# Kernel tuning notes

Hardware: AMD Instinct MI355X
Metric: run time of the kernel (lower is better)

Reference implementation:

```python
import jax, jax.numpy as jnp
import numpy as np

IN_FEATURES = 2048
OUT_FEATURES = 8192
HARMONICS = 256
TWO_PI = 2.0 * np.pi


def setup_inputs() -> dict:
    key = jax.random.key(0)
    kx, kb, kp = jax.random.split(key, 3)
    x = jax.random.normal(kx, (4, 4096, IN_FEATURES), dtype=jnp.float32)
    # basis: randn then L2-normalized along in_features (dim=1), as in torch buffer init
    basis = jax.random.normal(kb, (HARMONICS, IN_FEATURES), dtype=jnp.float32)
    basis = basis / jnp.linalg.norm(basis, axis=1, keepdims=True)
    phase = jax.random.normal(kp, (OUT_FEATURES, HARMONICS), dtype=jnp.float32) * TWO_PI
    amp = jnp.ones((OUT_FEATURES, HARMONICS), dtype=jnp.float32) / HARMONICS
    return {"x": x, "basis": basis, "phase": phase, "amp": amp}


def reference(x, basis, phase, amp):
    # resonance = x @ basis.T : [..., harmonics]
    resonance = jnp.einsum("bsi,hi->bsh", x, basis)
    # Real part of (resonance + 0i) * (amp*cos(phase) + i*amp*sin(phase)) summed over h
    # collapses to resonance @ (amp * cos(phase)).T -- identical math, no complex dtype.
    w_real = amp * jnp.cos(phase)  # [out, harmonics]
    return jnp.einsum("bsh,oh->bso", resonance, w_real)
```

## Files before the change

### kernel.cpp

```cpp
#include <hip/hip_runtime.h>
#include <hip/hip_bf16.h>
#include <stdint.h>
#include <stddef.h>


typedef __bf16 bf16x8 __attribute__((ext_vector_type(8)));
typedef float  f32x4  __attribute__((ext_vector_type(4)));
typedef float  f32x16 __attribute__((ext_vector_type(16)));
typedef unsigned short u16x8 __attribute__((ext_vector_type(8)));

#define M_ROWS 16384
#define K_IN   2048
#define N_OUT  8192
#define N_HARM 256

__device__ inline unsigned short f2bf(float f) {
    union { float f; uint32_t u; } c; c.f = f;
    uint32_t u = c.u;
    uint32_t r = (u + 0x7fffu + ((u >> 16) & 1u)) >> 16;
    return (unsigned short)r;
}

__device__ inline bf16x8 cvt8(f32x4 a, f32x4 b) {
    bf16x8 r;
    r[0] = (__bf16)a[0]; r[1] = (__bf16)a[1]; r[2] = (__bf16)a[2]; r[3] = (__bf16)a[3];
    r[4] = (__bf16)b[0]; r[5] = (__bf16)b[1]; r[6] = (__bf16)b[2]; r[7] = (__bf16)b[3];
    return r;
}

#define GLDS(src, dst) \
    __builtin_amdgcn_global_load_lds((const __attribute__((address_space(1))) void*)(src), \
                                     (__attribute__((address_space(3))) void*)(dst), 16, 0, 0)

__global__ __launch_bounds__(256) void cvt_bf16(const float* __restrict__ in,
                                                unsigned short* __restrict__ out) {
    size_t i = ((size_t)blockIdx.x * 256 + threadIdx.x) * 8;
    f32x4 v0 = *(const f32x4*)(in + i);
    f32x4 v1 = *(const f32x4*)(in + i + 4);
    u16x8 o;
    o[0] = f2bf(v0[0]); o[1] = f2bf(v0[1]); o[2] = f2bf(v0[2]); o[3] = f2bf(v0[3]);
    o[4] = f2bf(v1[0]); o[5] = f2bf(v1[1]); o[6] = f2bf(v1[2]); o[7] = f2bf(v1[3]);
    *(u16x8*)(out + i) = o;
}

__global__ __launch_bounds__(256) void wreal_bf16(const float* __restrict__ phase,
                                                  const float* __restrict__ amp,
                                                  unsigned short* __restrict__ out) {
    size_t i = ((size_t)blockIdx.x * 256 + threadIdx.x) * 8;
    f32x4 p0 = *(const f32x4*)(phase + i);
    f32x4 p1 = *(const f32x4*)(phase + i + 4);
    f32x4 a0 = *(const f32x4*)(amp + i);
    f32x4 a1 = *(const f32x4*)(amp + i + 4);
    u16x8 o;
    o[0] = f2bf(a0[0] * cosf(p0[0])); o[1] = f2bf(a0[1] * cosf(p0[1]));
    o[2] = f2bf(a0[2] * cosf(p0[2])); o[3] = f2bf(a0[3] * cosf(p0[3]));
    o[4] = f2bf(a1[0] * cosf(p1[0])); o[5] = f2bf(a1[1] * cosf(p1[1]));
    o[6] = f2bf(a1[2] * cosf(p1[2])); o[7] = f2bf(a1[3] * cosf(p1[3]));
    *(u16x8*)(out + i) = o;
}

__global__ __launch_bounds__(256) void gemm1_fused(const float* __restrict__ A,
                                                   const unsigned short* __restrict__ B,
                                                   unsigned short* __restrict__ C) {
    __shared__ float          Asm[2][32 * 64];
    __shared__ unsigned short Bsm[2][256 * 64];

    const int tid  = threadIdx.x;
    const int lane = tid & 63;
    const int wv   = tid >> 6;
    const int bm0  = blockIdx.x * 32;

    const float* srcA[2];
#pragma unroll
    for (int q = 0; q < 2; ++q) {
        int L = q * 256 + tid;
        int r = L >> 4, p = L & 15;
        int c = p ^ (r & 15);
        srcA[q] = A + (size_t)(bm0 + r) * K_IN + c * 4;
    }
    const unsigned short* srcB[8];
#pragma unroll
    for (int q = 0; q < 8; ++q) {
        int L = q * 256 + tid;
        int r = L >> 3, p = L & 7;
        int c = p ^ (r & 7);
        srcB[q] = B + (size_t)r * K_IN + c * 8;
    }
    const int dA = wv * 256 + lane * 4;
    const int dB = wv * 512 + lane * 8;

    f32x16 acc[2];
#pragma unroll
    for (int nf = 0; nf < 2; ++nf)
#pragma unroll
        for (int e = 0; e < 16; ++e) acc[nf][e] = 0.f;

    const int r   = lane & 31;
    const int g   = lane >> 5;
    const int r15 = r & 15;
    const int colb = wv * 64;

#pragma unroll
    for (int q = 0; q < 2; ++q) GLDS(srcA[q], &Asm[0][q * 1024 + dA]);
#pragma unroll
    for (int q = 0; q < 8; ++q) GLDS(srcB[q], &Bsm[0][q * 2048 + dB]);
    __syncthreads();

    for (int t = 0; t < 32; ++t) {
        const int buf = t & 1;
        if (t + 1 < 32) {
            const int k0 = (t + 1) * 64;
#pragma unroll
            for (int q = 0; q < 2; ++q) GLDS(srcA[q] + k0, &Asm[buf ^ 1][q * 1024 + dA]);
#pragma unroll
            for (int q = 0; q < 8; ++q) GLDS(srcB[q] + k0, &Bsm[buf ^ 1][q * 2048 + dB]);
        }

        bf16x8 af[4];
#pragma unroll
        for (int ks = 0; ks < 4; ++ks) {
            const int c0 = g * 2 + ks * 4;
            f32x4 lo = *(const f32x4*)&Asm[buf][r * 64 + ((c0)     ^ r15) * 4];
            f32x4 hi = *(const f32x4*)&Asm[buf][r * 64 + ((c0 + 1) ^ r15) * 4];
            af[ks] = cvt8(lo, hi);
        }
#pragma unroll
        for (int nf = 0; nf < 2; ++nf) {
            const int rB = colb + nf * 32 + r;
            const int r7 = rB & 7;
#pragma unroll
            for (int ks = 0; ks < 4; ++ks) {
                const int cB = g + ks * 2;
                bf16x8 bfrag = *(const bf16x8*)&Bsm[buf][rB * 64 + (cB ^ r7) * 8];
                acc[nf] = __builtin_amdgcn_mfma_f32_32x32x16_bf16(af[ks], bfrag, acc[nf], 0, 0, 0);
            }
        }
        __syncthreads();
    }

#pragma unroll
    for (int nf = 0; nf < 2; ++nf)
#pragma unroll
        for (int reg = 0; reg < 16; ++reg) {
            int row = bm0 + (reg & 3) + 8 * (reg >> 2) + 4 * g;
            int col = colb + nf * 32 + r;
            C[(size_t)row * N_HARM + col] = f2bf(acc[nf][reg]);
        }
}

template<int K, int NCOLS>
__global__ __launch_bounds__(256) void gemm_bt(const unsigned short* __restrict__ A,
                                               const unsigned short* __restrict__ B,
                                               float* __restrict__ Cv) {
    __shared__ unsigned short As[2][128 * 32];
    __shared__ unsigned short Bs[2][128 * 32];

    const int tid  = threadIdx.x;
    const int lane = tid & 63;
    const int wv   = tid >> 6;
    const int wr   = wv >> 1;
    const int wc   = wv & 1;
    const int bm0  = blockIdx.y * 128;
    const int bn0  = blockIdx.x * 128;

    const int srow = tid >> 2;
    const int scol = (tid & 3) * 8;
    const unsigned short* gA0 = A + (size_t)(bm0 + srow) * K + scol;
    const unsigned short* gA1 = gA0 + (size_t)64 * K;
    const unsigned short* gB0 = B + (size_t)(bn0 + srow) * K + scol;
    const unsigned short* gB1 = gB0 + (size_t)64 * K;
    const int dL0 = wv * 512 + (lane & 63) * 8;
    const int dL1 = 2048 + wv * 512 + (lane & 63) * 8;

    f32x4 acc[4][4];
#pragma unroll
    for (int i = 0; i < 4; ++i)
#pragma unroll
        for (int j = 0; j < 4; ++j) acc[i][j] = (f32x4){0.f, 0.f, 0.f, 0.f};

    const int frow = lane & 15;
    const int kseg = (lane >> 4) * 8;
    constexpr int NT = K / 32;

    GLDS(gA0, &As[0][dL0]); GLDS(gA1, &As[0][dL1]);
    GLDS(gB0, &Bs[0][dL0]); GLDS(gB1, &Bs[0][dL1]);
    __syncthreads();

    for (int t = 0; t < NT; ++t) {
        const int buf = t & 1;
        if (t + 1 < NT) {
            const int k0 = (t + 1) * 32;
            GLDS(gA0 + k0, &As[buf ^ 1][dL0]); GLDS(gA1 + k0, &As[buf ^ 1][dL1]);
            GLDS(gB0 + k0, &Bs[buf ^ 1][dL0]); GLDS(gB1 + k0, &Bs[buf ^ 1][dL1]);
        }

        bf16x8 af[4], bfr[4];
#pragma unroll
        for (int i = 0; i < 4; ++i) {
            af[i]  = *(const bf16x8*)(&As[buf][(wr * 64 + i * 16 + frow) * 32 + kseg]);
            bfr[i] = *(const bf16x8*)(&Bs[buf][(wc * 64 + i * 16 + frow) * 32 + kseg]);
        }
#pragma unroll
        for (int i = 0; i < 4; ++i)
#pragma unroll
            for (int j = 0; j < 4; ++j)
                acc[i][j] = __builtin_amdgcn_mfma_f32_16x16x32_bf16(af[i], bfr[j], acc[i][j], 0, 0, 0);

        __syncthreads();
    }

#pragma unroll
    for (int i = 0; i < 4; ++i)
#pragma unroll
        for (int j = 0; j < 4; ++j)
#pragma unroll
            for (int rg = 0; rg < 4; ++rg) {
                int row = bm0 + wr * 64 + i * 16 + (lane >> 4) * 4 + rg;
                int col = bn0 + wc * 64 + j * 16 + (lane & 15);
                Cv[(size_t)row * NCOLS + col] = acc[i][j][rg];
            }
}

extern "C" void kernel_launch(void* const* d_in, const int* in_sizes, int n_in,
                              void* d_out, int out_size, void* d_ws, size_t ws_size,
                              hipStream_t stream) {
    const float* x     = (const float*)d_in[0];
    const float* basis = (const float*)d_in[1];
    const float* phase = (const float*)d_in[2];
    const float* amp   = (const float*)d_in[3];
    float* out = (float*)d_out;

    char* ws = (char*)d_ws;
    unsigned short* bb  = (unsigned short*)(ws);
    unsigned short* wrb = (unsigned short*)(ws + 1048576);
    unsigned short* rb  = (unsigned short*)(ws + 5242880);

    cvt_bf16<<<dim3(256), dim3(256), 0, stream>>>(basis, bb);
    wreal_bf16<<<dim3(1024), dim3(256), 0, stream>>>(phase, amp, wrb);

    gemm1_fused<<<dim3(M_ROWS / 32), dim3(256), 0, stream>>>(x, bb, rb);
    gemm_bt<256, 8192><<<dim3(N_OUT / 128, M_ROWS / 128), dim3(256), 0, stream>>>(rb, wrb, out);
}
```

Before: 207.3 us.

## Restructure second GEMM to keep weight fragments in registers and stream rows

Replaces the tiled 128x128 second GEMM with a kernel where each wave holds a 32-column slice of the full K=256 weight matrix in registers and streams 32-row tiles of the resonance matrix through a triple-buffered, swizzled LDS ring. Each tile's output is written straight out after 16 MFMAs, so weight loads from LDS and repeated accumulator setup go away. The aim is to cut LDS traffic and keep the kernel bound by the fp32 output stores. The cost is 512-thread blocks with heavy register use, only 512 blocks in the grid, and a barrier after every store phase, which may limit how much memory traffic overlaps.

Result: faster. 188.5 us (-9.1%).

```diff
diff --git a/kernel.cpp b/kernel.cpp
--- a/kernel.cpp
+++ b/kernel.cpp
@@ -148,77 +148,70 @@
         }
 }
 
-template<int K, int NCOLS>
-__global__ __launch_bounds__(256) void gemm_bt(const unsigned short* __restrict__ A,
-                                               const unsigned short* __restrict__ B,
-                                               float* __restrict__ Cv) {
-    __shared__ unsigned short As[2][128 * 32];
-    __shared__ unsigned short Bs[2][128 * 32];
+__global__ __launch_bounds__(512) void gemm2_nstream(const unsigned short* __restrict__ A,
+                                                     const unsigned short* __restrict__ B,
+                                                     float* __restrict__ Cv) {
+    __shared__ unsigned short As[3][32 * 256];
 
     const int tid  = threadIdx.x;
     const int lane = tid & 63;
     const int wv   = tid >> 6;
-    const int wr   = wv >> 1;
-    const int wc   = wv & 1;
-    const int bm0  = blockIdx.y * 128;
-    const int bn0  = blockIdx.x * 128;
-
-    const int srow = tid >> 2;
-    const int scol = (tid & 3) * 8;
-    const unsigned short* gA0 = A + (size_t)(bm0 + srow) * K + scol;
-    const unsigned short* gA1 = gA0 + (size_t)64 * K;
-    const unsigned short* gB0 = B + (size_t)(bn0 + srow) * K + scol;
-    const unsigned short* gB1 = gB0 + (size_t)64 * K;
-    const int dL0 = wv * 512 + (lane & 63) * 8;
-    const int dL1 = 2048 + wv * 512 + (lane & 63) * 8;
-
-    f32x4 acc[4][4];
-#pragma unroll
-    for (int i = 0; i < 4; ++i)
-#pragma unroll
-        for (int j = 0; j < 4; ++j) acc[i][j] = (f32x4){0.f, 0.f, 0.f, 0.f};
-
-    const int frow = lane & 15;
-    const int kseg = (lane >> 4) * 8;
-    constexpr int NT = K / 32;
-
-    GLDS(gA0, &As[0][dL0]); GLDS(gA1, &As[0][dL1]);
-    GLDS(gB0, &Bs[0][dL0]); GLDS(gB1, &Bs[0][dL1]);
+    const int r    = lane & 31;
+    const int g    = lane >> 5;
+    const int r7   = r & 7;
+
+    const int col0  = blockIdx.x * 256 + wv * 32;
+    const int mbase = blockIdx.y * 1024;
+
+    bf16x8 bf[16];
+#pragma unroll
+    for (int ks = 0; ks < 16; ++ks)
+        bf[ks] = *(const bf16x8*)(B + (size_t)(col0 + r) * N_HARM + ks * 16 + g * 8);
+
+    const unsigned short* srcA[2];
+#pragma unroll
+    for (int q = 0; q < 2; ++q) {
+        int L = q * 512 + tid;
+        int row = L >> 5, slot = L & 31;
+        int c = slot ^ (row & 7);
+        srcA[q] = A + (size_t)(mbase + row) * N_HARM + c * 8;
+    }
+    const int dstA = tid * 8;
+
+    GLDS(srcA[0], &As[0][dstA]);
+    GLDS(srcA[1], &As[0][4096 + dstA]);
     __syncthreads();
 
-    for (int t = 0; t < NT; ++t) {
-        const int buf = t & 1;
-        if (t + 1 < NT) {
-            const int k0 = (t + 1) * 32;
-            GLDS(gA0 + k0, &As[buf ^ 1][dL0]); GLDS(gA1 + k0, &As[buf ^ 1][dL1]);
-            GLDS(gB0 + k0, &Bs[buf ^ 1][dL0]); GLDS(gB1 + k0, &Bs[buf ^ 1][dL1]);
-        }
-
-        bf16x8 af[4], bfr[4];
-#pragma unroll
-        for (int i = 0; i < 4; ++i) {
-            af[i]  = *(const bf16x8*)(&As[buf][(wr * 64 + i * 16 + frow) * 32 + kseg]);
-            bfr[i] = *(const bf16x8*)(&Bs[buf][(wc * 64 + i * 16 + frow) * 32 + kseg]);
-        }
-#pragma unroll
-        for (int i = 0; i < 4; ++i)
-#pragma unroll
-            for (int j = 0; j < 4; ++j)
-                acc[i][j] = __builtin_amdgcn_mfma_f32_16x16x32_bf16(af[i], bfr[j], acc[i][j], 0, 0, 0);
+    for (int t = 0; t < 32; ++t) {
+        const int cur = t % 3;
+        if (t + 1 < 32) {
+            const int nxt = (t + 1) % 3;
+            __builtin_amdgcn_sched_barrier(0);
+            GLDS(srcA[0] + (t + 1) * 32 * N_HARM, &As[nxt][dstA]);
+            GLDS(srcA[1] + (t + 1) * 32 * N_HARM, &As[nxt][4096 + dstA]);
+            __builtin_amdgcn_sched_barrier(0);
+        }
+
+        f32x16 acc;
+#pragma unroll
+        for (int e = 0; e < 16; ++e) acc[e] = 0.f;
+
+#pragma unroll
+        for (int ks = 0; ks < 16; ++ks) {
+            const int c = ks * 2 + g;
+            bf16x8 af = *(const bf16x8*)&As[cur][r * 256 + (c ^ r7) * 8];
+            acc = __builtin_amdgcn_mfma_f32_32x32x16_bf16(af, bf[ks], acc, 0, 0, 0);
+        }
+
+        const int m0 = mbase + t * 32;
+#pragma unroll
+        for (int reg = 0; reg < 16; ++reg) {
+            int row = m0 + (reg & 3) + 8 * (reg >> 2) + 4 * g;
+            Cv[(size_t)row * N_OUT + col0 + r] = acc[reg];
+        }
 
         __syncthreads();
     }
-
-#pragma unroll
-    for (int i = 0; i < 4; ++i)
-#pragma unroll
-        for (int j = 0; j < 4; ++j)
-#pragma unroll
-            for (int rg = 0; rg < 4; ++rg) {
-                int row = bm0 + wr * 64 + i * 16 + (lane >> 4) * 4 + rg;
-                int col = bn0 + wc * 64 + j * 16 + (lane & 15);
-                Cv[(size_t)row * NCOLS + col] = acc[i][j][rg];
-            }
 }
 
 extern "C" void kernel_launch(void* const* d_in, const int* in_sizes, int n_in,
@@ -239,5 +232,5 @@
     wreal_bf16<<<dim3(1024), dim3(256), 0, stream>>>(phase, amp, wrb);
 
     gemm1_fused<<<dim3(M_ROWS / 32), dim3(256), 0, stream>>>(x, bb, rb);
-    gemm_bt<256, 8192><<<dim3(N_OUT / 128, M_ROWS / 128), dim3(256), 0, stream>>>(rb, wrb, out);
-}
+    gemm2_nstream<<<dim3(32, 16), dim3(512), 0, stream>>>(rb, wrb, out);
+}
```
